# Optimization experiments

Measured on AMD Instinct MI355X. Metric: run time of the kernel, lower is better.

Reference implementation:

```python
import jax, jax.numpy as jnp
import numpy as np

N_NODES = 100000
N_EDGES = 1600000
IN_DIM = 128
HID = 128
OUT_DIM = 64
N_LAYERS = 3


def setup_inputs() -> dict:
    key = jax.random.key(0)
    ks = jax.random.split(key, 8)
    x = jax.random.normal(ks[0], (N_NODES, IN_DIM), dtype=jnp.float32)
    edge_index = jax.random.randint(ks[1], (2, N_EDGES), 0, N_NODES, dtype=jnp.int64)
    s = 1.0 / np.sqrt(HID)
    Wl = jax.random.normal(ks[2], (N_LAYERS, HID, HID), dtype=jnp.float32) * s
    Wr = jax.random.normal(ks[3], (N_LAYERS, HID, HID), dtype=jnp.float32) * s
    b = jnp.zeros((N_LAYERS, HID), dtype=jnp.float32)
    fc_w = jax.random.normal(ks[4], (N_LAYERS * HID, OUT_DIM), dtype=jnp.float32) * (1.0 / np.sqrt(N_LAYERS * HID))
    fc_b = jnp.zeros((OUT_DIM,), dtype=jnp.float32)
    return {"x": x, "edge_index": edge_index, "Wl": Wl, "Wr": Wr, "b": b, "fc_w": fc_w, "fc_b": fc_b}


def _sage_conv(x, src, dst, Wl, Wr, b, n_nodes):
    # PyG SAGEConv (aggr='mean'): out = lin_l(mean_{j->i} x_j) + lin_r(x_i)
    msg = x[src]                                             # [E, d] gather
    agg = jax.ops.segment_sum(msg, dst, num_segments=n_nodes)  # [N, d]
    deg = jax.ops.segment_sum(jnp.ones((src.shape[0],), x.dtype), dst, num_segments=n_nodes)
    mean = agg / jnp.maximum(deg, 1.0)[:, None]
    return mean @ Wl + x @ Wr + b


def reference(x, edge_index, Wl, Wr, b, fc_w, fc_b):
    src, dst = edge_index[0], edge_index[1]
    n = x.shape[0]
    h = x
    layer_out = []
    for i in range(N_LAYERS):  # small fixed layer count
        h = jax.nn.relu(_sage_conv(h, src, dst, Wl[i], Wr[i], b[i], n))
        layer_out.append(h)  # dropout p=0 -> identity
    hk = jnp.concatenate(layer_out, axis=-1)  # JK 'cat': [N, L*HID]
    return hk @ fc_w + fc_b
```

## Files before the change

### kernel.cpp

```cpp
#include <hip/hip_runtime.h>
#include <hip/hip_bf16.h>
#include <stdint.h>

#define N_NODES 100000
#define N_EDGES 1600000
#define HID 128
#define OUT_DIM 64
#define N_LAYERS 3
#define CAP 64
#define CAP_SHIFT 6
#define BIN_SHIFT 12
#define NBIN ((N_NODES + (1 << BIN_SHIFT) - 1) >> BIN_SHIFT)
#define EPT 4

typedef __attribute__((ext_vector_type(8))) short short8;
typedef __attribute__((ext_vector_type(4))) float v4f;
typedef __attribute__((ext_vector_type(4))) unsigned short ushort4v;

__device__ __forceinline__ float bf2f(unsigned int lo16) {
    union { unsigned int i; float f; } v; v.i = lo16 << 16; return v.f;
}
__device__ __forceinline__ unsigned short f2bf(float f) {
    union { float f; unsigned int i; } v; v.f = f;
    unsigned int r = v.i + 0x7fffu + ((v.i >> 16) & 1u);
    return (unsigned short)(r >> 16);
}

__device__ __forceinline__ void stage16(const void* g, void* l) {
    __builtin_amdgcn_global_load_lds(
        (const __attribute__((address_space(1))) unsigned int*)g,
        (__attribute__((address_space(3))) unsigned int*)l, 16, 0, 0);
}

#define CONV_N (N_NODES * HID / 4)
__global__ void prologue(const int* __restrict__ raw, int* __restrict__ flag,
                         int* __restrict__ cursor,
                         const float* __restrict__ x, unsigned short* __restrict__ xb,
                         const float* __restrict__ Wl, const float* __restrict__ Wr,
                         const float* __restrict__ fc_w,
                         unsigned short* __restrict__ WlT, unsigned short* __restrict__ WrT,
                         unsigned short* __restrict__ fcT) {
    int gidx = blockIdx.x * blockDim.x + threadIdx.x;
    if (blockIdx.x == 0 && threadIdx.x < 64) {
        int v = raw[2 * threadIdx.x + 1];
        unsigned long long b = __ballot(v != 0);
        if (threadIdx.x == 0) *flag = (b == 0ull) ? 1 : 0;
    }
    if (gidx < N_NODES) cursor[gidx] = gidx << CAP_SHIFT;

    if (gidx < CONV_N) {
        float4 v = ((const float4*)x)[gidx];
        ushort4v o;
        o[0] = f2bf(v.x); o[1] = f2bf(v.y); o[2] = f2bf(v.z); o[3] = f2bf(v.w);
        ((ushort4v*)xb)[gidx] = o;
        return;
    }
    int idx = gidx - CONV_N;
    const int WELEMS = N_LAYERS * HID * HID;
    if (idx < WELEMS) {
        int l = idx / (HID * HID);
        int rem = idx - l * HID * HID;
        int k = rem / HID, nn2 = rem - k * HID;
        WlT[l * HID * HID + nn2 * HID + k] = f2bf(Wl[idx]);
        WrT[l * HID * HID + nn2 * HID + k] = f2bf(Wr[idx]);
    } else {
        int j = idx - WELEMS;
        if (j < N_LAYERS * HID * OUT_DIM) {
            int l = j / (HID * OUT_DIM);
            int rem = j - l * HID * OUT_DIM;
            int k = rem / OUT_DIM, o = rem - k * OUT_DIM;
            fcT[l * OUT_DIM * HID + o * HID + k] = f2bf(fc_w[(l * HID + k) * OUT_DIM + o]);
        }
    }
}

__global__ __launch_bounds__(256) void fill_ell(const int* __restrict__ raw,
                                                const int* __restrict__ flag,
                                                int* __restrict__ cursor,
                                                int* __restrict__ ell) {
    int e0 = blockIdx.x * (256 * EPT) + threadIdx.x;
    int s[EPT], d[EPT], bin[EPT];
    bool is64 = (*flag != 0);
#pragma unroll
    for (int k = 0; k < EPT; ++k) {
        int e = e0 + k * 256;
        if (e < N_EDGES) {
            if (is64) {
                const long long* r = (const long long*)raw;
                d[k] = (int)r[N_EDGES + e];
                s[k] = (int)r[e];
            } else {
                d[k] = raw[N_EDGES + e];
                s[k] = raw[e];
            }
            bin[k] = d[k] >> BIN_SHIFT;
        } else {
            bin[k] = 0x7fffffff;
        }
    }
#pragma unroll 1
    for (int p = 0; p < NBIN; ++p) {
#pragma unroll
        for (int k = 0; k < EPT; ++k) {
            if (bin[k] == p) {
                int pos = atomicAdd(&cursor[d[k]], 1);
                if (pos < ((d[k] + 1) << CAP_SHIFT)) ell[pos] = s[k];
            }
        }
    }
}

__global__ void finalize_deg(const int* __restrict__ cursor, int* __restrict__ deg,
                             float* __restrict__ inv_deg, int* __restrict__ ell,
                             unsigned short* b0, unsigned short* b1,
                             unsigned short* b2) {
    int i = blockIdx.x * blockDim.x + threadIdx.x;
    if (i < N_NODES) {
        int d = cursor[i] - (i << CAP_SHIFT);
        if (d > CAP) d = CAP;
        deg[i] = d;
        inv_deg[i] = 1.0f / (float)(d > 0 ? d : 1);
        int r = (d + 7) & ~7;
        int base = i << CAP_SHIFT;
        for (int p = d; p < r; ++p) ell[base + p] = N_NODES;
    }
    if (blockIdx.x == 0 && threadIdx.x < 192) {
        int t = threadIdx.x;
        unsigned short* bufs[3] = {b0, b1, b2};
        uint32_t* p = (uint32_t*)bufs[t >> 6];
        p[(size_t)N_NODES * 64 + (t & 63)] = 0;
    }
}

__global__ __launch_bounds__(256) void agg_bf(
    const unsigned short* __restrict__ h, const int* __restrict__ ell,
    const int* __restrict__ deg, const float* __restrict__ inv_deg,
    unsigned short* __restrict__ meanb) {
    int tid = threadIdx.x;
    int grp = tid >> 4;
    int lane16 = tid & 15;
    int node = blockIdx.x * 16 + grp;
    bool valid = node < N_NODES;
    int nd = valid ? node : 0;
    int dg = valid ? deg[nd] : 0;
    int dgp = (dg + 7) & ~7;
    int base = nd << CAP_SHIFT;
    const uint4* hv = (const uint4*)h;
    float a[8];
#pragma unroll
    for (int c = 0; c < 8; ++c) a[c] = 0.f;

    for (int t = 0; t < dgp; t += 8) {
        int idx[8];
#pragma unroll
        for (int u = 0; u < 8; ++u) idx[u] = ell[base + t + u];
        uint4 v[8];
#pragma unroll
        for (int u = 0; u < 8; ++u) v[u] = hv[(size_t)idx[u] * 16 + lane16];
#pragma unroll
        for (int u = 0; u < 8; ++u) {
            a[0] += bf2f(v[u].x & 0xffffu); a[1] += bf2f(v[u].x >> 16);
            a[2] += bf2f(v[u].y & 0xffffu); a[3] += bf2f(v[u].y >> 16);
            a[4] += bf2f(v[u].z & 0xffffu); a[5] += bf2f(v[u].z >> 16);
            a[6] += bf2f(v[u].w & 0xffffu); a[7] += bf2f(v[u].w >> 16);
        }
    }
    if (valid) {
        float id = inv_deg[nd];
        uint4 o;
        o.x = (uint32_t)f2bf(a[0] * id) | ((uint32_t)f2bf(a[1] * id) << 16);
        o.y = (uint32_t)f2bf(a[2] * id) | ((uint32_t)f2bf(a[3] * id) << 16);
        o.z = (uint32_t)f2bf(a[4] * id) | ((uint32_t)f2bf(a[5] * id) << 16);
        o.w = (uint32_t)f2bf(a[6] * id) | ((uint32_t)f2bf(a[7] * id) << 16);
        *(uint4*)&meanb[(size_t)node * HID + lane16 * 8] = o;
    }
}

__global__ __launch_bounds__(256, 2) void layer_mfma(
    const unsigned short* __restrict__ Am,
    const unsigned short* __restrict__ Ah,
    const unsigned short* __restrict__ WlT,
    const unsigned short* __restrict__ WrT,
    const float* __restrict__ bias,
    unsigned short* __restrict__ Hout, int n) {
    __shared__ uint4 smA[128 * 16];
    __shared__ uint4 smB[128 * 16];
    int tid = threadIdx.x;
    int w = tid >> 6, L = tid & 63;
    int q = L >> 4, r16 = L & 15;
    int colbase = (w & 1) * 64;
    int nodebase = (w >> 1) * 64;
    int node0 = blockIdx.x * 128;

    {
        const unsigned short* srcs[2] = {Am, Ah};
#pragma unroll
        for (int op = 0; op < 2; ++op) {
            const unsigned short* S = srcs[op];
            char* D = (char*)(op ? smB : smA);
#pragma unroll
            for (int i = 0; i < 8; ++i) {
                int c = (w << 3) + i;
                int row_l = (c << 2) + (L >> 4);
                int chunk = (L & 15) ^ (row_l & 7);
                const unsigned short* src =
                    S + (((size_t)(node0 + row_l)) << 7) + (chunk << 3);
                stage16(src, D + (c << 10));
            }
        }
    }

    short8 wfr[2][4][4];
#pragma unroll
    for (int seg = 0; seg < 2; ++seg) {
        const unsigned short* WT = seg ? WrT : WlT;
#pragma unroll
        for (int t = 0; t < 4; ++t)
#pragma unroll
            for (int i = 0; i < 4; ++i)
                wfr[seg][t][i] =
                    *(const short8*)&WT[(colbase + i * 16 + r16) * HID + t * 32 + q * 8];
    }

    __syncthreads();

    v4f acc[4][4];
#pragma unroll
    for (int i = 0; i < 4; ++i)
#pragma unroll
        for (int j = 0; j < 4; ++j)
#pragma unroll
            for (int r = 0; r < 4; ++r) acc[i][j][r] = 0.f;

#pragma unroll
    for (int seg = 0; seg < 2; ++seg) {
        const uint4* SM = seg ? smB : smA;
#pragma unroll
        for (int t = 0; t < 4; ++t) {
            short8 bfr[4];
#pragma unroll
            for (int j = 0; j < 4; ++j) {
                int row = nodebase + j * 16 + r16;
                bfr[j] = *(const short8*)&SM[(row << 4) + ((t * 4 + q) ^ (row & 7))];
            }
#pragma unroll
            for (int i = 0; i < 4; ++i)
#pragma unroll
                for (int j = 0; j < 4; ++j)
                    acc[i][j] = __builtin_amdgcn_mfma_f32_16x16x32_bf16(
                        wfr[seg][t][i], bfr[j], acc[i][j], 0, 0, 0);
        }
    }

#pragma unroll
    for (int i = 0; i < 4; ++i) {
        int col = colbase + i * 16 + q * 4;
        float4 bv = *(const float4*)&bias[col];
#pragma unroll
        for (int j = 0; j < 4; ++j) {
            int node = node0 + nodebase + j * 16 + r16;
            if (node < n) {
                float v0 = acc[i][j][0] + bv.x;
                float v1 = acc[i][j][1] + bv.y;
                float v2 = acc[i][j][2] + bv.z;
                float v3 = acc[i][j][3] + bv.w;
                ushort4v o;
                o[0] = f2bf(v0 > 0.f ? v0 : 0.f);
                o[1] = f2bf(v1 > 0.f ? v1 : 0.f);
                o[2] = f2bf(v2 > 0.f ? v2 : 0.f);
                o[3] = f2bf(v3 > 0.f ? v3 : 0.f);
                *(ushort4v*)&Hout[(size_t)node * HID + col] = o;
            }
        }
    }
}

__global__ __launch_bounds__(256, 2) void layer3_fc(
    const unsigned short* __restrict__ Am,
    const unsigned short* __restrict__ Ah,
    const unsigned short* __restrict__ WlT,
    const unsigned short* __restrict__ WrT,
    const float* __restrict__ bias,
    const unsigned short* __restrict__ hA,
    const unsigned short* __restrict__ fcT,
    const float* __restrict__ fc_b,
    float* __restrict__ out, int n) {
    __shared__ uint4 smA[128 * 16];
    __shared__ uint4 smB[128 * 16];
    int tid = threadIdx.x;
    int w = tid >> 6, L = tid & 63;
    int q = L >> 4, r16 = L & 15;
    int colbase = (w & 1) * 64;
    int nodebase = (w >> 1) * 64;
    int node0 = blockIdx.x * 128;

    {
        const unsigned short* srcs[2] = {Am, Ah};
#pragma unroll
        for (int op = 0; op < 2; ++op) {
            const unsigned short* S = srcs[op];
            char* D = (char*)(op ? smB : smA);
#pragma unroll
            for (int i = 0; i < 8; ++i) {
                int c = (w << 3) + i;
                int row_l = (c << 2) + (L >> 4);
                int chunk = (L & 15) ^ (row_l & 7);
                const unsigned short* src =
                    S + (((size_t)(node0 + row_l)) << 7) + (chunk << 3);
                stage16(src, D + (c << 10));
            }
        }
    }

    short8 wfr[2][4][4];
#pragma unroll
    for (int seg = 0; seg < 2; ++seg) {
        const unsigned short* WT = seg ? WrT : WlT;
#pragma unroll
        for (int t = 0; t < 4; ++t)
#pragma unroll
            for (int i = 0; i < 4; ++i)
                wfr[seg][t][i] =
                    *(const short8*)&WT[(colbase + i * 16 + r16) * HID + t * 32 + q * 8];
    }

    __syncthreads();

    v4f acc[4][4];
#pragma unroll
    for (int i = 0; i < 4; ++i)
#pragma unroll
        for (int j = 0; j < 4; ++j)
#pragma unroll
            for (int r = 0; r < 4; ++r) acc[i][j][r] = 0.f;

#pragma unroll
    for (int seg = 0; seg < 2; ++seg) {
        const uint4* SM = seg ? smB : smA;
#pragma unroll
        for (int t = 0; t < 4; ++t) {
            short8 bfr[4];
#pragma unroll
            for (int j = 0; j < 4; ++j) {
                int row = nodebase + j * 16 + r16;
                bfr[j] = *(const short8*)&SM[(row << 4) + ((t * 4 + q) ^ (row & 7))];
            }
#pragma unroll
            for (int i = 0; i < 4; ++i)
#pragma unroll
                for (int j = 0; j < 4; ++j)
                    acc[i][j] = __builtin_amdgcn_mfma_f32_16x16x32_bf16(
                        wfr[seg][t][i], bfr[j], acc[i][j], 0, 0, 0);
        }
    }

    int nd2[2], gvalid[2];
#pragma unroll
    for (int j = 0; j < 2; ++j) {
        int t = node0 + w * 32 + j * 16 + r16;
        gvalid[j] = t < n;
        nd2[j] = gvalid[j] ? t : n - 1;
    }
    short8 ha[2][4];
#pragma unroll
    for (int j = 0; j < 2; ++j)
#pragma unroll
        for (int t = 0; t < 4; ++t)
            ha[j][t] = *(const short8*)&hA[(size_t)nd2[j] * HID + t * 32 + q * 8];

    __syncthreads();

#pragma unroll
    for (int i = 0; i < 4; ++i) {
        int col = colbase + i * 16 + q * 4;
        float4 bv = *(const float4*)&bias[col];
#pragma unroll
        for (int j = 0; j < 4; ++j) {
            int row = nodebase + j * 16 + r16;
            float v0 = acc[i][j][0] + bv.x;
            float v1 = acc[i][j][1] + bv.y;
            float v2 = acc[i][j][2] + bv.z;
            float v3 = acc[i][j][3] + bv.w;
            uint2 val;
            val.x = (uint32_t)f2bf(v0 > 0.f ? v0 : 0.f) |
                    ((uint32_t)f2bf(v1 > 0.f ? v1 : 0.f) << 16);
            val.y = (uint32_t)f2bf(v2 > 0.f ? v2 : 0.f) |
                    ((uint32_t)f2bf(v3 > 0.f ? v3 : 0.f) << 16);
            int slot = (col >> 3) ^ (row & 7);
            uint2* p2 = (uint2*)&smA[(row << 4) + slot];
            p2[q & 1] = val;
        }
    }
    __syncthreads();

    v4f acc2[4][2];
#pragma unroll
    for (int i = 0; i < 4; ++i) {
        float4 bv = *(const float4*)&fc_b[i * 16 + q * 4];
#pragma unroll
        for (int j = 0; j < 2; ++j) {
            acc2[i][j][0] = bv.x; acc2[i][j][1] = bv.y;
            acc2[i][j][2] = bv.z; acc2[i][j][3] = bv.w;
        }
    }

#pragma unroll
    for (int l = 0; l < 3; ++l) {
        const unsigned short* F = fcT + (size_t)l * OUT_DIM * HID;
#pragma unroll
        for (int t = 0; t < 4; ++t) {
            int koff = t * 32 + q * 8;
            short8 afr[4], bfr[2];
#pragma unroll
            for (int i = 0; i < 4; ++i)
                afr[i] = *(const short8*)&F[(i * 16 + r16) * HID + koff];
#pragma unroll
            for (int j = 0; j < 2; ++j) {
                int row = w * 32 + j * 16 + r16;
                if (l == 0)
                    bfr[j] = ha[j][t];
                else if (l == 1)
                    bfr[j] = *(const short8*)&smB[(row << 4) + ((t * 4 + q) ^ (row & 7))];
                else
                    bfr[j] = *(const short8*)&smA[(row << 4) + ((t * 4 + q) ^ (row & 7))];
            }
#pragma unroll
            for (int i = 0; i < 4; ++i)
#pragma unroll
                for (int j = 0; j < 2; ++j)
                    acc2[i][j] = __builtin_amdgcn_mfma_f32_16x16x32_bf16(afr[i], bfr[j], acc2[i][j], 0, 0, 0);
        }
    }

#pragma unroll
    for (int i = 0; i < 4; ++i)
#pragma unroll
        for (int j = 0; j < 2; ++j)
            if (gvalid[j])
                *(v4f*)&out[(size_t)nd2[j] * OUT_DIM + i * 16 + q * 4] = acc2[i][j];
}

extern "C" void kernel_launch(void* const* d_in, const int* in_sizes, int n_in,
                              void* d_out, int out_size, void* d_ws, size_t ws_size,
                              hipStream_t stream) {
    const float* x     = (const float*)d_in[0];
    const int*   edges = (const int*)d_in[1];
    const float* Wl    = (const float*)d_in[2];
    const float* Wr    = (const float*)d_in[3];
    const float* b     = (const float*)d_in[4];
    const float* fc_w  = (const float*)d_in[5];
    const float* fc_b  = (const float*)d_in[6];
    float* out = (float*)d_out;

    char* ws = (char*)d_ws;
    size_t off = 0;
    auto alloc = [&](size_t bytes) {
        void* p = ws + off;
        off = (off + bytes + 255) & ~(size_t)255;
        return p;
    };
    int*   flag    = (int*)alloc(256);
    int*   cursor  = (int*)alloc((size_t)N_NODES * 4);
    int*   deg     = (int*)alloc((size_t)N_NODES * 4);
    float* inv_deg = (float*)alloc((size_t)N_NODES * 4);
    int*   ell     = (int*)alloc(((size_t)N_NODES * CAP + 64) * 4);
    unsigned short* xb    = (unsigned short*)alloc((size_t)(N_NODES + 128) * HID * 2);
    unsigned short* meanb = (unsigned short*)alloc((size_t)(N_NODES + 128) * HID * 2);
    unsigned short* hA    = (unsigned short*)alloc((size_t)(N_NODES + 128) * HID * 2);
    unsigned short* hB    = (unsigned short*)alloc((size_t)(N_NODES + 128) * HID * 2);
    unsigned short* WlT   = (unsigned short*)alloc((size_t)N_LAYERS * HID * HID * 2);
    unsigned short* WrT   = (unsigned short*)alloc((size_t)N_LAYERS * HID * HID * 2);
    unsigned short* fcT   = (unsigned short*)alloc((size_t)N_LAYERS * OUT_DIM * HID * 2);

    const int PREP_TOTAL = CONV_N + N_LAYERS * HID * HID + N_LAYERS * HID * OUT_DIM;
    prologue<<<(PREP_TOTAL + 255) / 256, 256, 0, stream>>>(
        edges, flag, cursor, x, xb, Wl, Wr, fc_w, WlT, WrT, fcT);
    fill_ell<<<(N_EDGES + 256 * EPT - 1) / (256 * EPT), 256, 0, stream>>>(
        edges, flag, cursor, ell);
    finalize_deg<<<(N_NODES + 255) / 256, 256, 0, stream>>>(cursor, deg, inv_deg, ell, xb, hA, hB);

    int ngrid = (N_NODES + 127) / 128;
    int agrid = (N_NODES + 15) / 16;

    agg_bf<<<agrid, 256, 0, stream>>>(xb, ell, deg, inv_deg, meanb);
    layer_mfma<<<ngrid, 256, 0, stream>>>(
        meanb, xb, WlT, WrT, b, hA, N_NODES);

    agg_bf<<<agrid, 256, 0, stream>>>(hA, ell, deg, inv_deg, meanb);
    layer_mfma<<<ngrid, 256, 0, stream>>>(
        meanb, hA, WlT + (size_t)HID * HID, WrT + (size_t)HID * HID, b + HID, hB, N_NODES);

    agg_bf<<<agrid, 256, 0, stream>>>(hB, ell, deg, inv_deg, meanb);
    layer3_fc<<<ngrid, 256, 0, stream>>>(
        meanb, hB, WlT + (size_t)2 * HID * HID, WrT + (size_t)2 * HID * HID, b + 2 * HID,
        hA, fcT, fc_b, out, N_NODES);
}
```

Baseline: 480.7 us.

## Build ELL adjacency via two-pass binned partition with shared-memory per-bin assembly

Replaces per-edge global atomic cursor inserts into the ELL table with a two-pass scheme. The first pass partitions edges into 256-node bins using shared-memory histograms and one global atomic per bin per block. The second pass builds each bin's ELL tile, degree and padding in shared memory and writes it out with coalesced stores. This targets scattered global atomics and uncoalesced ELL writes, at the cost of an intermediate bins buffer with a fixed per-bin cap (8192) and a 64KB shared tile that limits occupancy. Edge order within a node's row becomes nondeterministic, which can change the bf16 aggregation summation order.

```diff
diff --git a/kernel.cpp b/kernel.cpp
--- a/kernel.cpp
+++ b/kernel.cpp
@@ -9,9 +9,10 @@
 #define N_LAYERS 3
 #define CAP 64
 #define CAP_SHIFT 6
-#define BIN_SHIFT 12
-#define NBIN ((N_NODES + (1 << BIN_SHIFT) - 1) >> BIN_SHIFT)
-#define EPT 4
+#define BIN_NODES 256
+#define NBIN2 ((N_NODES + BIN_NODES - 1) / BIN_NODES)
+#define BINCAP 8192
+#define EPT 8
 
 typedef __attribute__((ext_vector_type(8))) short short8;
 typedef __attribute__((ext_vector_type(4))) float v4f;
@@ -34,19 +35,26 @@
 
 #define CONV_N (N_NODES * HID / 4)
 __global__ void prologue(const int* __restrict__ raw, int* __restrict__ flag,
-                         int* __restrict__ cursor,
+                         int* __restrict__ bin_cnt,
                          const float* __restrict__ x, unsigned short* __restrict__ xb,
                          const float* __restrict__ Wl, const float* __restrict__ Wr,
                          const float* __restrict__ fc_w,
                          unsigned short* __restrict__ WlT, unsigned short* __restrict__ WrT,
-                         unsigned short* __restrict__ fcT) {
+                         unsigned short* __restrict__ fcT,
+                         unsigned short* b0, unsigned short* b1, unsigned short* b2) {
     int gidx = blockIdx.x * blockDim.x + threadIdx.x;
     if (blockIdx.x == 0 && threadIdx.x < 64) {
         int v = raw[2 * threadIdx.x + 1];
         unsigned long long b = __ballot(v != 0);
         if (threadIdx.x == 0) *flag = (b == 0ull) ? 1 : 0;
     }
-    if (gidx < N_NODES) cursor[gidx] = gidx << CAP_SHIFT;
+    if (gidx < NBIN2) bin_cnt[gidx] = 0;
+    if (blockIdx.x == 1 && threadIdx.x < 192) {
+        int t = threadIdx.x;
+        unsigned short* bufs[3] = {b0, b1, b2};
+        uint32_t* p = (uint32_t*)bufs[t >> 6];
+        p[(size_t)N_NODES * 64 + (t & 63)] = 0;
+    }
 
     if (gidx < CONV_N) {
         float4 v = ((const float4*)x)[gidx];
@@ -74,12 +82,18 @@
     }
 }
 
-__global__ __launch_bounds__(256) void fill_ell(const int* __restrict__ raw,
-                                                const int* __restrict__ flag,
-                                                int* __restrict__ cursor,
-                                                int* __restrict__ ell) {
-    int e0 = blockIdx.x * (256 * EPT) + threadIdx.x;
-    int s[EPT], d[EPT], bin[EPT];
+__global__ __launch_bounds__(256) void fill_p1(const int* __restrict__ raw,
+                                               const int* __restrict__ flag,
+                                               int* __restrict__ bin_cnt,
+                                               unsigned int* __restrict__ bins) {
+    __shared__ int h[NBIN2];
+    __shared__ int basekeep[NBIN2];
+    int tid = threadIdx.x;
+    for (int b = tid; b < NBIN2; b += 256) h[b] = 0;
+    __syncthreads();
+
+    int e0 = blockIdx.x * (256 * EPT) + tid;
+    int s[EPT], d[EPT];
     bool is64 = (*flag != 0);
 #pragma unroll
     for (int k = 0; k < EPT; ++k) {
@@ -93,42 +107,73 @@
                 d[k] = raw[N_EDGES + e];
                 s[k] = raw[e];
             }
-            bin[k] = d[k] >> BIN_SHIFT;
         } else {
-            bin[k] = 0x7fffffff;
-        }
-    }
-#pragma unroll 1
-    for (int p = 0; p < NBIN; ++p) {
-#pragma unroll
-        for (int k = 0; k < EPT; ++k) {
-            if (bin[k] == p) {
-                int pos = atomicAdd(&cursor[d[k]], 1);
-                if (pos < ((d[k] + 1) << CAP_SHIFT)) ell[pos] = s[k];
-            }
-        }
-    }
-}
-
-__global__ void finalize_deg(const int* __restrict__ cursor, int* __restrict__ deg,
-                             float* __restrict__ inv_deg, int* __restrict__ ell,
-                             unsigned short* b0, unsigned short* b1,
-                             unsigned short* b2) {
-    int i = blockIdx.x * blockDim.x + threadIdx.x;
-    if (i < N_NODES) {
-        int d = cursor[i] - (i << CAP_SHIFT);
-        if (d > CAP) d = CAP;
-        deg[i] = d;
-        inv_deg[i] = 1.0f / (float)(d > 0 ? d : 1);
-        int r = (d + 7) & ~7;
-        int base = i << CAP_SHIFT;
-        for (int p = d; p < r; ++p) ell[base + p] = N_NODES;
-    }
-    if (blockIdx.x == 0 && threadIdx.x < 192) {
-        int t = threadIdx.x;
-        unsigned short* bufs[3] = {b0, b1, b2};
-        uint32_t* p = (uint32_t*)bufs[t >> 6];
-        p[(size_t)N_NODES * 64 + (t & 63)] = 0;
+            d[k] = -1;
+        }
+    }
+#pragma unroll
+    for (int k = 0; k < EPT; ++k)
+        if (d[k] >= 0) atomicAdd(&h[d[k] >> 8], 1);
+    __syncthreads();
+    for (int b = tid; b < NBIN2; b += 256) {
+        int c = h[b];
+        basekeep[b] = c ? atomicAdd(&bin_cnt[b], c) : 0;
+        h[b] = 0;
+    }
+    __syncthreads();
+#pragma unroll
+    for (int k = 0; k < EPT; ++k) {
+        if (d[k] >= 0) {
+            int b = d[k] >> 8;
+            int off = basekeep[b] + atomicAdd(&h[b], 1);
+            if (off < BINCAP)
+                bins[(size_t)b * BINCAP + off] =
+                    ((unsigned int)s[k] << 8) | (unsigned int)(d[k] & 255);
+        }
+    }
+}
+
+__global__ __launch_bounds__(256) void fill_p2(const int* __restrict__ bin_cnt,
+                                               const unsigned int* __restrict__ bins,
+                                               int* __restrict__ ell,
+                                               int* __restrict__ deg,
+                                               float* __restrict__ inv_deg, int n) {
+    __shared__ int tile[BIN_NODES * CAP];
+    __shared__ int cnt[BIN_NODES];
+    int b = blockIdx.x, tid = threadIdx.x;
+    for (int i = tid; i < BIN_NODES; i += 256) cnt[i] = 0;
+    __syncthreads();
+
+    int m = bin_cnt[b];
+    if (m > BINCAP) m = BINCAP;
+    for (int i = tid; i < m; i += 256) {
+        unsigned int e = bins[(size_t)b * BINCAP + i];
+        int dl = (int)(e & 255u);
+        int slot = atomicAdd(&cnt[dl], 1);
+        if (slot < CAP) tile[(dl << CAP_SHIFT) + slot] = (int)(e >> 8);
+    }
+    __syncthreads();
+
+    int node0 = b << 8;
+    for (int i = tid; i < BIN_NODES; i += 256) {
+        int node = node0 + i;
+        if (node < n) {
+            int dgf = cnt[i];
+            int dg = dgf > CAP ? CAP : dgf;
+            deg[node] = dg;
+            inv_deg[node] = 1.0f / (float)(dg > 0 ? dg : 1);
+            int r = (dg + 7) & ~7;
+            for (int p = dg; p < r; ++p) tile[(i << CAP_SHIFT) + p] = N_NODES;
+        }
+    }
+    __syncthreads();
+
+    const uint4* t4 = (const uint4*)tile;
+    uint4* g4 = (uint4*)ell;
+    for (int v = tid; v < BIN_NODES * 16; v += 256) {
+        int row = v >> 4;
+        int node = node0 + row;
+        if (node < n) g4[((size_t)node << 4) + (v & 15)] = t4[v];
     }
 }
 
@@ -460,10 +505,11 @@
         return p;
     };
     int*   flag    = (int*)alloc(256);
-    int*   cursor  = (int*)alloc((size_t)N_NODES * 4);
+    int*   bin_cnt = (int*)alloc((size_t)NBIN2 * 4);
     int*   deg     = (int*)alloc((size_t)N_NODES * 4);
     float* inv_deg = (float*)alloc((size_t)N_NODES * 4);
     int*   ell     = (int*)alloc(((size_t)N_NODES * CAP + 64) * 4);
+    unsigned int* bins = (unsigned int*)alloc((size_t)NBIN2 * BINCAP * 4);
     unsigned short* xb    = (unsigned short*)alloc((size_t)(N_NODES + 128) * HID * 2);
     unsigned short* meanb = (unsigned short*)alloc((size_t)(N_NODES + 128) * HID * 2);
     unsigned short* hA    = (unsigned short*)alloc((size_t)(N_NODES + 128) * HID * 2);
@@ -474,10 +520,10 @@
 
     const int PREP_TOTAL = CONV_N + N_LAYERS * HID * HID + N_LAYERS * HID * OUT_DIM;
     prologue<<<(PREP_TOTAL + 255) / 256, 256, 0, stream>>>(
-        edges, flag, cursor, x, xb, Wl, Wr, fc_w, WlT, WrT, fcT);
-    fill_ell<<<(N_EDGES + 256 * EPT - 1) / (256 * EPT), 256, 0, stream>>>(
-        edges, flag, cursor, ell);
-    finalize_deg<<<(N_NODES + 255) / 256, 256, 0, stream>>>(cursor, deg, inv_deg, ell, xb, hA, hB);
+        edges, flag, bin_cnt, x, xb, Wl, Wr, fc_w, WlT, WrT, fcT, xb, hA, hB);
+    fill_p1<<<(N_EDGES + 256 * EPT - 1) / (256 * EPT), 256, 0, stream>>>(
+        edges, flag, bin_cnt, bins);
+    fill_p2<<<NBIN2, 256, 0, stream>>>(bin_cnt, bins, ell, deg, inv_deg, N_NODES);
 
     int ngrid = (N_NODES + 127) / 128;
     int agrid = (N_NODES + 15) / 16;
```

New measurement: 438.9 us. -8.7%, faster.
